# Kernel tuning notes

Hardware: AMD Instinct MI355X
Metric: run time of the kernel (lower is better)

The kernel has to match this reference:

```python
import jax, jax.numpy as jnp
import numpy as np

D_MODEL = 1024
N_HEADS = 16
HEAD_DIM = D_MODEL // N_HEADS  # 64, rope_dim == head_dim
D_FF = 4096
BATCH = 2
SEQ = 2048
EPS = 1e-6


def setup_inputs() -> dict:
    key = jax.random.key(0)
    ks = jax.random.split(key, 12)
    x = jax.random.normal(ks[0], (BATCH, SEQ, D_MODEL), dtype=jnp.float32)
    # realistic RoPE angles: theta = pos * inv_freq, duplicated to fill rope_dim
    half = HEAD_DIM // 2
    inv_freq = 1.0 / (10000.0 ** (jnp.arange(0, half, dtype=jnp.float32) / half))
    pos = jnp.arange(SEQ, dtype=jnp.float32)
    freqs = pos[:, None] * inv_freq[None, :]              # [S, half]
    rotary_pos_emb = jnp.concatenate([freqs, freqs], axis=-1)[:, None, :]  # [S,1,64]
    s = D_MODEL ** -0.5
    wq = jax.random.normal(ks[1], (D_MODEL, D_MODEL), dtype=jnp.float32) * s
    wk = jax.random.normal(ks[2], (D_MODEL, D_MODEL), dtype=jnp.float32) * s
    wv = jax.random.normal(ks[3], (D_MODEL, D_MODEL), dtype=jnp.float32) * s
    wo = jax.random.normal(ks[4], (D_MODEL, D_MODEL), dtype=jnp.float32) * s
    w_gate = jax.random.normal(ks[5], (D_FF, D_MODEL), dtype=jnp.float32) * s
    w_up = jax.random.normal(ks[6], (D_FF, D_MODEL), dtype=jnp.float32) * s
    w_down = jax.random.normal(ks[7], (D_MODEL, D_FF), dtype=jnp.float32) * (D_FF ** -0.5)
    norm1_w = jnp.ones((D_MODEL,), dtype=jnp.float32)
    norm2_w = jnp.ones((D_MODEL,), dtype=jnp.float32)
    return {"x": x, "rotary_pos_emb": rotary_pos_emb, "wq": wq, "wk": wk,
            "wv": wv, "wo": wo, "w_gate": w_gate, "w_up": w_up,
            "w_down": w_down, "norm1_w": norm1_w, "norm2_w": norm2_w}


def _rms_norm(x, w):
    # torch: x / (||x||/sqrt(d) + eps) * w  (eps added to the norm, not variance)
    norm = jnp.linalg.norm(x, axis=-1, keepdims=True) * (x.shape[-1] ** -0.5)
    return x / (norm + EPS) * w


def _rotate_half(t):
    t1, t2 = jnp.split(t, 2, axis=-1)
    return jnp.concatenate([-t2, t1], axis=-1)


def _apply_rope(t, cos, sin):
    # t: [B,H,S,D]; cos/sin: [S,D] broadcast over batch/heads
    return t * cos[None, None] + _rotate_half(t) * sin[None, None]


def reference(x, rotary_pos_emb, wq, wk, wv, wo, w_gate, w_up, w_down, norm1_w, norm2_w):
    B, S, _ = x.shape
    H, D = N_HEADS, HEAD_DIM

    # ---- attention sublayer ----
    residual = x
    h = _rms_norm(x, norm1_w)
    q = (h @ wq.T).reshape(B, S, H, D).transpose(0, 2, 1, 3)  # [B,H,S,D]
    k = (h @ wk.T).reshape(B, S, H, D).transpose(0, 2, 1, 3)
    v = (h @ wv.T).reshape(B, S, H, D).transpose(0, 2, 1, 3)

    freqs = rotary_pos_emb[:, 0, :]  # [S, D] (rope_dim == head_dim)
    cos, sin = jnp.cos(freqs), jnp.sin(freqs)
    q = _apply_rope(q, cos, sin)
    k = _apply_rope(k, cos, sin)

    scores = jnp.einsum('bhsd,bhtd->bhst', q, k) / jnp.sqrt(jnp.float32(D))
    causal = jnp.tril(jnp.ones((S, S), dtype=bool))  # True = keep
    scores = jnp.where(causal[None, None], scores, jnp.finfo(scores.dtype).min)
    attn = jax.nn.softmax(scores, axis=-1)  # dropout is identity in eval
    attn_out = jnp.einsum('bhst,bhtd->bhsd', attn, v)
    attn_out = attn_out.transpose(0, 2, 1, 3).reshape(B, S, H * D)
    x = residual + attn_out @ wo.T

    # ---- SwiGLU MLP sublayer ----
    residual = x
    h = _rms_norm(x, norm2_w)
    gate = h @ w_gate.T
    up = h @ w_up.T
    ff = (jax.nn.silu(gate) * up) @ w_down.T
    return residual + ff
```

## Files before the change

kernel.cpp:

```cpp
#include <hip/hip_runtime.h>

typedef __bf16 bf16;
typedef __attribute__((ext_vector_type(8))) __bf16 bf16x8;
typedef __attribute__((ext_vector_type(4))) float f32x4;

#define B_SZ 2
#define SEQ 2048
#define DM 1024
#define NH 16
#define HD 64
#define DFF 4096
#define NROWS (B_SZ*SEQ)

__device__ __forceinline__ f32x4 mfma16(bf16x8 a, bf16x8 b, f32x4 c) {
    return __builtin_amdgcn_mfma_f32_16x16x32_bf16(a, b, c, 0, 0, 0);
}

__device__ __forceinline__ void gload16(const bf16* g, bf16* l) {
    __builtin_amdgcn_global_load_lds(
        (const __attribute__((address_space(1))) void*)g,
        (__attribute__((address_space(3))) void*)l, 16, 0, 0);
}


__global__ __launch_bounds__(256) void convert_all_k(
    const float* __restrict__ wq, const float* __restrict__ wk,
    const float* __restrict__ wv, const float* __restrict__ wo,
    const float* __restrict__ wg, const float* __restrict__ wu,
    const float* __restrict__ wd,
    bf16* __restrict__ wqkvb, bf16* __restrict__ wob,
    bf16* __restrict__ wgub, bf16* __restrict__ wdb) {
    const long M1 = 1l << 20;
    long i = ((long)blockIdx.x * 256 + threadIdx.x) * 8;
    const float* src; bf16* dst; long off;
    if (i < 3 * M1) {
        int sct = (int)(i >> 20);
        src = sct == 0 ? wq : (sct == 1 ? wk : wv);
        off = i & (M1 - 1); dst = wqkvb + i;
    } else if (i < 4 * M1) {
        src = wo; off = i - 3 * M1; dst = wob + off;
    } else if (i < 12 * M1) {
        long j = i - 4 * M1;
        int fr = (int)(j >> 10), c = (int)(j & 1023);
        int b = fr >> 8, half = (fr >> 7) & 1, f = (b << 7) | (fr & 127);
        src = half ? wu : wg; off = (long)f * 1024 + c; dst = wgub + j;
    } else {
        src = wd; off = i - 12 * M1; dst = wdb + off;
    }
    float4 v0 = *(const float4*)(src + off);
    float4 v1 = *(const float4*)(src + off + 4);
    dst[0] = (bf16)v0.x; dst[1] = (bf16)v0.y; dst[2] = (bf16)v0.z; dst[3] = (bf16)v0.w;
    dst[4] = (bf16)v1.x; dst[5] = (bf16)v1.y; dst[6] = (bf16)v1.z; dst[7] = (bf16)v1.w;
}

__global__ __launch_bounds__(256) void rope_table_k(const float* __restrict__ rope,
                                                    float* __restrict__ ct,
                                                    float* __restrict__ st) {
    int i = blockIdx.x * 256 + threadIdx.x;
    int sI = i >> 5, d = i & 31;
    float f = rope[sI * 64 + d];
    ct[i] = cosf(f);
    st[i] = sinf(f);
}

__global__ __launch_bounds__(256) void rmsnorm_k(const float* __restrict__ x,
                                                 const float* __restrict__ w,
                                                 bf16* __restrict__ o) {
    int row = blockIdx.x;
    int tid = threadIdx.x;
    float4 v = ((const float4*)(x + (long)row * DM))[tid];
    float ss = v.x*v.x + v.y*v.y + v.z*v.z + v.w*v.w;
    #pragma unroll
    for (int off = 32; off >= 1; off >>= 1) ss += __shfl_xor(ss, off, 64);
    __shared__ float sred[4];
    if ((tid & 63) == 0) sred[tid >> 6] = ss;
    __syncthreads();
    float tot = sred[0] + sred[1] + sred[2] + sred[3];
    float scale = 1.f / (sqrtf(tot * (1.f / (float)DM)) + 1e-6f);
    float4 wv = ((const float4*)w)[tid];
    bf16* orow = o + (long)row * DM + tid * 4;
    orow[0] = (bf16)(v.x * scale * wv.x);
    orow[1] = (bf16)(v.y * scale * wv.y);
    orow[2] = (bf16)(v.z * scale * wv.z);
    orow[3] = (bf16)(v.w * scale * wv.w);
}


template<int EPI>
__global__ __launch_bounds__(512, 2)
void gemm256(const bf16* __restrict__ A, const bf16* __restrict__ W,
             int K, bf16* __restrict__ o1, bf16* __restrict__ o2,
             bf16* __restrict__ o3,
             const float* __restrict__ ct, const float* __restrict__ st) {
    __shared__ __align__(16) char smem[131072];
    bf16* Ah = (bf16*)smem;
    bf16* Bh = (bf16*)(smem + 65536);
    const int tid = threadIdx.x;
    const int wid = tid >> 6, l = tid & 63;
    const int lr = l & 15, lg = l >> 4;
    const int wr = wid >> 2, wcn = wid & 3;
    const int nwg = gridDim.x * gridDim.y;
    const int orig = blockIdx.y * gridDim.x + blockIdx.x;
    const int swz = (orig & 7) * (nwg >> 3) + (orig >> 3);
    const int bx = swz % gridDim.x, by = swz / gridDim.x;
    const long mbase = (long)bx * 256;
    const long nbase = (long)by * 256;

    f32x4 acc[8][4] = {};
    const int nk = K >> 6;
    const int P = nk * 2;

    const int aoff0 = lr * 64 + ((wr * 4 + lg) ^ (lr & 7)) * 8;
    const int boff0 = ((wcn & 1) * 64 + lr) * 64 + (((wcn >> 1) * 4 + lg) ^ (lr & 7)) * 8;

    auto stageHalf = [&](int ph) {
        const int d = (ph >> 1) & 1, h = ph & 1, kt = ph >> 1;
        bf16* abase = Ah + (d * 2 + h) * 8192;
        bf16* bbase = Bh + (d * 2 + h) * 8192;
        const long kcol = (long)kt * 64 + h * 32;
        #pragma unroll
        for (int i = 0; i < 2; ++i) {
            int s = i * 512 + tid;
            int prow = s >> 3, pblk = s & 7;
            int L = pblk ^ (prow & 7);
            long gr = (long)((L >> 2) * 128 + prow);
            long gc = kcol + (L & 3) * 8;
            gload16(&A[(mbase + gr) * K + gc], abase + s * 8);
            gload16(&W[(nbase + gr) * K + gc], bbase + s * 8);
        }
    };

    auto computeHalf = [&](int ph) {
        const int d = (ph >> 1) & 1, h = ph & 1;
        const bf16* abase = Ah + (d * 2 + h) * 8192;
        const bf16* bbase = Bh + (d * 2 + h) * 8192;
        bf16x8 bfr[4];
        #pragma unroll
        for (int ni = 0; ni < 4; ++ni)
            bfr[ni] = *(const bf16x8*)&bbase[ni * 1024 + boff0];
        #pragma unroll
        for (int ms = 0; ms < 2; ++ms) {
            bf16x8 af[4];
            #pragma unroll
            for (int mi = 0; mi < 4; ++mi)
                af[mi] = *(const bf16x8*)&abase[(ms * 4 + mi) * 1024 + aoff0];
            __builtin_amdgcn_s_setprio(1);
            #pragma unroll
            for (int mi = 0; mi < 4; ++mi)
                #pragma unroll
                for (int ni = 0; ni < 4; ++ni)
                    acc[ms * 4 + mi][ni] = mfma16(af[mi], bfr[ni], acc[ms * 4 + mi][ni]);
            __builtin_amdgcn_s_setprio(0);
        }
    };

    stageHalf(0);
    stageHalf(1);
    for (int p = 0; p < P; ++p) {
        if (p + 2 < P) stageHalf(p + 2);
        if (p < P - 2)       asm volatile("s_waitcnt vmcnt(8)" ::: "memory");
        else if (p == P - 2) asm volatile("s_waitcnt vmcnt(4)" ::: "memory");
        else                 asm volatile("s_waitcnt vmcnt(0)" ::: "memory");
        __builtin_amdgcn_s_barrier();
        __builtin_amdgcn_sched_barrier(0);
        computeHalf(p);
    }

    if (EPI == 0) {
        const long colW = nbase + wcn * 64;
        const int sect = (int)(colW >> 10);
        const int hh = (int)((colW >> 6) & 15);
        #pragma unroll
        for (int a = 0; a < 8; ++a) {
            #pragma unroll
            for (int nn = 0; nn < 2; ++nn) {
                const int dd = nn * 16 + lr;
                #pragma unroll
                for (int r = 0; r < 4; ++r) {
                    long row = mbase + wr * 128 + a * 16 + 4 * lg + r;
                    int b = (int)(row >> 11), s = (int)(row & 2047);
                    float v1 = acc[a][nn][r];
                    float v2 = acc[a][nn + 2][r];
                    if (sect < 2) {
                        float c = ct[s * 32 + dd], sn = st[s * 32 + dd];
                        bf16* dst = (sect == 0) ? o1 : o2;
                        long pth = (((long)(b * NH + hh) * SEQ + s) << 6) + dd;
                        dst[pth]      = (bf16)(v1 * c - v2 * sn);
                        dst[pth + 32] = (bf16)(v2 * c + v1 * sn);
                    } else {
                        long pth = ((long)(b * NH + hh) * HD + dd) * SEQ + s;
                        o3[pth]            = (bf16)v1;
                        o3[pth + 32 * SEQ] = (bf16)v2;
                    }
                }
            }
        }
    }

    if (EPI == 3) {
        const int fbase = (int)(nbase >> 1);
        bf16* Gl = (bf16*)smem;
        __syncthreads();
        if (wcn < 2) {
            #pragma unroll
            for (int a = 0; a < 8; ++a)
                #pragma unroll
                for (int ni = 0; ni < 4; ++ni)
                    #pragma unroll
                    for (int r = 0; r < 4; ++r) {
                        int grow = wr * 128 + a * 16 + 4 * lg + r;
                        int fc = wcn * 64 + ni * 16 + lr;
                        Gl[grow * 132 + fc] = (bf16)acc[a][ni][r];
                    }
        }
        __syncthreads();
        if (wcn >= 2) {
            #pragma unroll
            for (int a = 0; a < 8; ++a)
                #pragma unroll
                for (int ni = 0; ni < 4; ++ni)
                    #pragma unroll
                    for (int r = 0; r < 4; ++r) {
                        int grow = wr * 128 + a * 16 + 4 * lg + r;
                        int fc = (wcn - 2) * 64 + ni * 16 + lr;
                        float g = (float)Gl[grow * 132 + fc];
                        float u = acc[a][ni][r];
                        float sg = g / (1.f + __expf(-g));
                        long row = mbase + grow;
                        o1[row * 4096 + fbase + fc] = (bf16)(sg * u);
                    }
        }
    }
}


__global__ __launch_bounds__(512, 4)
void gemm64x128(const bf16* __restrict__ A, const bf16* __restrict__ W,
                int K, int N, const float* __restrict__ resid, float* __restrict__ of) {
    __shared__ bf16 As[2][64 * 64];
    __shared__ bf16 Bs[2][128 * 64];
    const int tid = threadIdx.x;
    const int wid = tid >> 6, l = tid & 63;
    const int lr = l & 15, lg = l >> 4;
    const int wr = wid >> 2, wcn = wid & 3;
    const long mbase = (long)blockIdx.x * 64;
    const long nbase = (long)blockIdx.y * 128;

    f32x4 acc[2][2] = {};
    const int nk = K >> 6;

    auto stage = [&](int b, int kt) {
        {
            int s = tid;
            int row = s >> 3, c8 = (s & 7) << 3;
            gload16(&A[(mbase + row) * K + kt * 64 + c8], &As[b][s * 8]);
        }
        #pragma unroll
        for (int i = 0; i < 2; ++i) {
            int s = i * 512 + tid;
            int row = s >> 3, c8 = (s & 7) << 3;
            gload16(&W[(nbase + row) * K + kt * 64 + c8], &Bs[b][s * 8]);
        }
    };
    auto compute = [&](int b) {
        #pragma unroll
        for (int kk = 0; kk < 2; ++kk) {
            bf16x8 af[2], bfr[2];
            #pragma unroll
            for (int mi = 0; mi < 2; ++mi)
                af[mi] = *(const bf16x8*)&As[b][(wr * 32 + mi * 16 + lr) * 64 + kk * 32 + lg * 8];
            #pragma unroll
            for (int ni = 0; ni < 2; ++ni)
                bfr[ni] = *(const bf16x8*)&Bs[b][(wcn * 32 + ni * 16 + lr) * 64 + kk * 32 + lg * 8];
            #pragma unroll
            for (int mi = 0; mi < 2; ++mi)
                #pragma unroll
                for (int ni = 0; ni < 2; ++ni)
                    acc[mi][ni] = mfma16(af[mi], bfr[ni], acc[mi][ni]);
        }
    };

    stage(0, 0);
    __syncthreads();
    int cur = 0;
    for (int kt = 0; kt < nk - 1; ++kt) {
        stage(cur ^ 1, kt + 1);
        compute(cur);
        __syncthreads();
        cur ^= 1;
    }
    compute(cur);

    #pragma unroll
    for (int mi = 0; mi < 2; ++mi)
        #pragma unroll
        for (int ni = 0; ni < 2; ++ni)
            #pragma unroll
            for (int r = 0; r < 4; ++r) {
                long row = mbase + wr * 32 + mi * 16 + 4 * lg + r;
                long col = nbase + wcn * 32 + ni * 16 + lr;
                of[row * N + col] = resid[row * N + col] + acc[mi][ni][r];
            }
}


__device__ __forceinline__ void attn_tile(
    int tb, int qw, bool diag,
    const bf16x8& qf0, const bf16x8& qf1,
    const bf16* Kl, const bf16* Vl, bf16* Plw,
    int lr, int lg, f32x4* oacc, float* mr, f32x4& lacc)
{
    f32x4 s[4];
    __builtin_amdgcn_s_setprio(1);
    #pragma unroll
    for (int tf = 0; tf < 4; ++tf) {
        f32x4 z = {0.f, 0.f, 0.f, 0.f};
        bf16x8 k0 = *(const bf16x8*)&Kl[(tf * 16 + lr) * 64 + ((0 + lg) ^ (lr & 7)) * 8];
        bf16x8 k1 = *(const bf16x8*)&Kl[(tf * 16 + lr) * 64 + ((4 + lg) ^ (lr & 7)) * 8];
        z = mfma16(qf0, k0, z);
        z = mfma16(qf1, k1, z);
        s[tf] = z;
    }
    __builtin_amdgcn_s_setprio(0);

    float pv[4][4];
    float pmax[4] = {-1e30f, -1e30f, -1e30f, -1e30f};
    #pragma unroll
    for (int tf = 0; tf < 4; ++tf) {
        int t = tb + tf * 16 + lr;
        #pragma unroll
        for (int r = 0; r < 4; ++r) {
            float sv = s[tf][r] * 0.125f;
            if (diag && t > qw + 4 * lg + r) sv = -1e30f;
            pv[tf][r] = sv;
            pmax[r] = fmaxf(pmax[r], sv);
        }
    }
    #pragma unroll
    for (int r = 0; r < 4; ++r) {
        pmax[r] = fmaxf(pmax[r], __shfl_xor(pmax[r], 8, 64));
        pmax[r] = fmaxf(pmax[r], __shfl_xor(pmax[r], 4, 64));
        pmax[r] = fmaxf(pmax[r], __shfl_xor(pmax[r], 2, 64));
        pmax[r] = fmaxf(pmax[r], __shfl_xor(pmax[r], 1, 64));
    }
    float alpha[4];
    #pragma unroll
    for (int r = 0; r < 4; ++r) {
        float mn = fmaxf(mr[r], pmax[r]);
        alpha[r] = __expf(mr[r] - mn);
        mr[r] = mn;
    }
    #pragma unroll
    for (int tf = 0; tf < 4; ++tf)
        #pragma unroll
        for (int r = 0; r < 4; ++r)
            Plw[(4 * lg + r) * 68 + tf * 16 + lr] = (bf16)__expf(pv[tf][r] - mr[r]);

    #pragma unroll
    for (int r = 0; r < 4; ++r) lacc[r] *= alpha[r];
    #pragma unroll
    for (int df = 0; df < 4; ++df) {
        f32x4 t4 = oacc[df];
        t4[0] *= alpha[0]; t4[1] *= alpha[1];
        t4[2] *= alpha[2]; t4[3] *= alpha[3];
        oacc[df] = t4;
    }
    bf16x8 pa0, pa1;
    #pragma unroll
    for (int j = 0; j < 8; ++j) {
        pa0[j] = Plw[lr * 68 + lg * 8 + j];
        pa1[j] = Plw[lr * 68 + 32 + lg * 8 + j];
    }
    bf16x8 ones;
    #pragma unroll
    for (int j = 0; j < 8; ++j) ones[j] = (bf16)1.0f;
    __builtin_amdgcn_s_setprio(1);
    lacc = mfma16(pa0, ones, lacc);
    lacc = mfma16(pa1, ones, lacc);
    #pragma unroll
    for (int df = 0; df < 4; ++df) {
        bf16x8 v0 = *(const bf16x8*)&Vl[(df * 16 + lr) * 64 + ((0 + lg) ^ (lr & 7)) * 8];
        bf16x8 v1 = *(const bf16x8*)&Vl[(df * 16 + lr) * 64 + ((4 + lg) ^ (lr & 7)) * 8];
        oacc[df] = mfma16(pa0, v0, oacc[df]);
        oacc[df] = mfma16(pa1, v1, oacc[df]);
    }
    __builtin_amdgcn_s_setprio(0);
}

__global__ __launch_bounds__(256)
void attn_fwd(const bf16* __restrict__ q, const bf16* __restrict__ k,
              const bf16* __restrict__ vt, bf16* __restrict__ o) {
    __shared__ bf16 Kl[2][64 * 64];
    __shared__ bf16 Vl[2][64 * 64];
    __shared__ bf16 Pl[4][16 * 68];
    const int tid = threadIdx.x, wid = tid >> 6, l = tid & 63;
    const int lr = l & 15, lg = l >> 4;
    const int qtA = blockIdx.x;
    const int qtB = 31 - qtA;
    const int bh = blockIdx.y;
    const long kbase = (long)bh * SEQ * HD;
    const long vbase = (long)bh * HD * SEQ;
    const int qwA = qtA * 64 + wid * 16;
    const int qwB = qtB * 64 + wid * 16;

    bf16x8 qA0, qA1, qB0, qB1;
    {
        const bf16* qp = q + kbase + (long)(qwA + lr) * HD + lg * 8;
        qA0 = *(const bf16x8*)qp; qA1 = *(const bf16x8*)(qp + 32);
        const bf16* qp2 = q + kbase + (long)(qwB + lr) * HD + lg * 8;
        qB0 = *(const bf16x8*)qp2; qB1 = *(const bf16x8*)(qp2 + 32);
    }
    f32x4 oA[4] = {}, oB[4] = {};
    f32x4 lA = {0.f, 0.f, 0.f, 0.f}, lB = {0.f, 0.f, 0.f, 0.f};
    float mA[4] = {-1e30f, -1e30f, -1e30f, -1e30f};
    float mB[4] = {-1e30f, -1e30f, -1e30f, -1e30f};

    auto stageKV = [&](int b, int tb) {
        #pragma unroll
        for (int i = 0; i < 4; ++i) {
            int slot = i * 256 + tid;
            int row = (slot >> 3) & 63;
            int bs = (slot & 7) ^ (row & 7);
            if (slot < 512)
                gload16(&k[kbase + (long)(tb + row) * HD + bs * 8], &Kl[b][slot * 8]);
            else
                gload16(&vt[vbase + (long)row * SEQ + tb + bs * 8], &Vl[b][(slot - 512) * 8]);
        }
    };

    const int nt = qtB + 1;
    stageKV(0, 0);
    __syncthreads();
    int cur = 0;
    for (int tb_i = 0; tb_i < nt; ++tb_i) {
        const int tb = tb_i * 64;
        if (tb_i + 1 < nt) stageKV(cur ^ 1, tb + 64);
        if (tb_i <= qtA)
            attn_tile(tb, qwA, tb_i == qtA, qA0, qA1, Kl[cur], Vl[cur], Pl[wid], lr, lg, oA, mA, lA);
        attn_tile(tb, qwB, tb_i == qtB, qB0, qB1, Kl[cur], Vl[cur], Pl[wid], lr, lg, oB, mB, lB);
        __syncthreads();
        cur ^= 1;
    }

    const int b = bh >> 4, h = bh & 15;
    #pragma unroll
    for (int df = 0; df < 4; ++df) {
        #pragma unroll
        for (int r = 0; r < 4; ++r) {
            int sA = qwA + 4 * lg + r;
            int sB = qwB + 4 * lg + r;
            o[((long)(b * SEQ + sA) * DM) + h * HD + df * 16 + lr] = (bf16)(oA[df][r] / lA[r]);
            o[((long)(b * SEQ + sB) * DM) + h * HD + df * 16 + lr] = (bf16)(oB[df][r] / lB[r]);
        }
    }
}


extern "C" void kernel_launch(void* const* d_in, const int* in_sizes, int n_in,
                              void* d_out, int out_size, void* d_ws, size_t ws_size,
                              hipStream_t stream) {
    (void)in_sizes; (void)n_in; (void)out_size; (void)ws_size;
    const float* x    = (const float*)d_in[0];
    const float* rope = (const float*)d_in[1];
    const float* wq   = (const float*)d_in[2];
    const float* wk   = (const float*)d_in[3];
    const float* wv   = (const float*)d_in[4];
    const float* wo   = (const float*)d_in[5];
    const float* wg   = (const float*)d_in[6];
    const float* wu   = (const float*)d_in[7];
    const float* wd   = (const float*)d_in[8];
    const float* n1w  = (const float*)d_in[9];
    const float* n2w  = (const float*)d_in[10];
    float* out = (float*)d_out;

    char* ws = (char*)d_ws;
    const size_t MB = 1u << 20;
    bf16* wqkvb = (bf16*)(ws + 0 * MB);
    bf16* wob   = (bf16*)(ws + 6 * MB);
    bf16* wgub  = (bf16*)(ws + 8 * MB);
    bf16* wdb   = (bf16*)(ws + 24 * MB);
    bf16* hb    = (bf16*)(ws + 32 * MB);
    bf16* qb_   = (bf16*)(ws + 40 * MB);
    bf16* kb_   = (bf16*)(ws + 56 * MB);
    bf16* vtb   = (bf16*)(ws + 72 * MB);
    bf16* attnb = (bf16*)(ws + 88 * MB);
    float* x2   = (float*)(ws + 40 * MB);
    bf16* midb  = (bf16*)(ws + 56 * MB);
    float* ctab = (float*)(ws + 104 * MB);
    float* stab = (float*)(ws + 104 * MB + (1u << 18));

    convert_all_k<<<8192, 256, 0, stream>>>(wq, wk, wv, wo, wg, wu, wd,
                                            wqkvb, wob, wgub, wdb);
    rope_table_k<<<256, 256, 0, stream>>>(rope, ctab, stab);

    rmsnorm_k<<<NROWS, 256, 0, stream>>>(x, n1w, hb);

    gemm256<0><<<dim3(16, 12), 512, 0, stream>>>(hb, wqkvb, DM, qb_, kb_, vtb, ctab, stab);

    attn_fwd<<<dim3(16, 32), 256, 0, stream>>>(qb_, kb_, vtb, attnb);

    gemm64x128<<<dim3(64, 8), 512, 0, stream>>>(attnb, wob, DM, DM, x, x2);

    rmsnorm_k<<<NROWS, 256, 0, stream>>>(x2, n2w, hb);

    gemm256<3><<<dim3(16, 32), 512, 0, stream>>>(hb, wgub, DM, midb, nullptr, nullptr, nullptr, nullptr);

    gemm64x128<<<dim3(64, 8), 512, 0, stream>>>(midb, wdb, DFF, DM, x2, out);
}
```

Baseline: 331.8 us.

## Deepen GEMM pipelines, swizzle LDS in small GEMM, interleave gate/up rows

The big GEMM moves from a 2-ahead to a 3-ahead staging of K half-tiles across four LDS buffers, issuing the next load after the barrier. The gate/up weight packing is re-interleaved in 32-row groups so each wave holds matching gate and up columns, which lets the SwiGLU epilogue run in registers without the LDS round-trip and two syncthreads. The 64x128 GEMM gains a triple-buffered LDS pipeline with explicit vmcnt waits, an XOR-swizzled LDS layout to cut bank conflicts, and setprio around the MFMAs. These changes raise LDS use and rely on hand-counted vmcnt values being correct.

```diff
diff --git a/kernel.cpp b/kernel.cpp
--- a/kernel.cpp
+++ b/kernel.cpp
@@ -42,8 +42,9 @@
     } else if (i < 12 * M1) {
         long j = i - 4 * M1;
         int fr = (int)(j >> 10), c = (int)(j & 1023);
-        int b = fr >> 8, half = (fr >> 7) & 1, f = (b << 7) | (fr & 127);
-        src = half ? wu : wg; off = (long)f * 1024 + c; dst = wgub + j;
+        int g = fr >> 6, r = fr & 63;
+        int f = g * 32 + (r & 31);
+        src = (r & 32) ? wu : wg; off = (long)f * 1024 + c; dst = wgub + j;
     } else {
         src = wd; off = i - 12 * M1; dst = wdb + off;
     }
@@ -114,9 +115,9 @@
     const int boff0 = ((wcn & 1) * 64 + lr) * 64 + (((wcn >> 1) * 4 + lg) ^ (lr & 7)) * 8;
 
     auto stageHalf = [&](int ph) {
-        const int d = (ph >> 1) & 1, h = ph & 1, kt = ph >> 1;
-        bf16* abase = Ah + (d * 2 + h) * 8192;
-        bf16* bbase = Bh + (d * 2 + h) * 8192;
+        const int buf = ph & 3, h = ph & 1, kt = ph >> 1;
+        bf16* abase = Ah + buf * 8192;
+        bf16* bbase = Bh + buf * 8192;
         const long kcol = (long)kt * 64 + h * 32;
         #pragma unroll
         for (int i = 0; i < 2; ++i) {
@@ -131,9 +132,9 @@
     };
 
     auto computeHalf = [&](int ph) {
-        const int d = (ph >> 1) & 1, h = ph & 1;
-        const bf16* abase = Ah + (d * 2 + h) * 8192;
-        const bf16* bbase = Bh + (d * 2 + h) * 8192;
+        const int buf = ph & 3;
+        const bf16* abase = Ah + buf * 8192;
+        const bf16* bbase = Bh + buf * 8192;
         bf16x8 bfr[4];
         #pragma unroll
         for (int ni = 0; ni < 4; ++ni)
@@ -156,13 +157,14 @@
 
     stageHalf(0);
     stageHalf(1);
+    stageHalf(2);
     for (int p = 0; p < P; ++p) {
-        if (p + 2 < P) stageHalf(p + 2);
         if (p < P - 2)       asm volatile("s_waitcnt vmcnt(8)" ::: "memory");
         else if (p == P - 2) asm volatile("s_waitcnt vmcnt(4)" ::: "memory");
         else                 asm volatile("s_waitcnt vmcnt(0)" ::: "memory");
         __builtin_amdgcn_s_barrier();
         __builtin_amdgcn_sched_barrier(0);
+        if (p + 3 < P) stageHalf(p + 3);
         computeHalf(p);
     }
 
@@ -198,38 +200,19 @@
     }
 
     if (EPI == 3) {
-        const int fbase = (int)(nbase >> 1);
-        bf16* Gl = (bf16*)smem;
-        __syncthreads();
-        if (wcn < 2) {
-            #pragma unroll
-            for (int a = 0; a < 8; ++a)
+        const int fb = (int)(nbase + wcn * 64) >> 1;
+        #pragma unroll
+        for (int a = 0; a < 8; ++a)
+            #pragma unroll
+            for (int ni = 0; ni < 2; ++ni)
                 #pragma unroll
-                for (int ni = 0; ni < 4; ++ni)
-                    #pragma unroll
-                    for (int r = 0; r < 4; ++r) {
-                        int grow = wr * 128 + a * 16 + 4 * lg + r;
-                        int fc = wcn * 64 + ni * 16 + lr;
-                        Gl[grow * 132 + fc] = (bf16)acc[a][ni][r];
-                    }
-        }
-        __syncthreads();
-        if (wcn >= 2) {
-            #pragma unroll
-            for (int a = 0; a < 8; ++a)
-                #pragma unroll
-                for (int ni = 0; ni < 4; ++ni)
-                    #pragma unroll
-                    for (int r = 0; r < 4; ++r) {
-                        int grow = wr * 128 + a * 16 + 4 * lg + r;
-                        int fc = (wcn - 2) * 64 + ni * 16 + lr;
-                        float g = (float)Gl[grow * 132 + fc];
-                        float u = acc[a][ni][r];
-                        float sg = g / (1.f + __expf(-g));
-                        long row = mbase + grow;
-                        o1[row * 4096 + fbase + fc] = (bf16)(sg * u);
-                    }
-        }
+                for (int r = 0; r < 4; ++r) {
+                    long row = mbase + wr * 128 + a * 16 + 4 * lg + r;
+                    float g = acc[a][ni][r];
+                    float u = acc[a][ni + 2][r];
+                    float sg = g / (1.f + __expf(-g));
+                    o1[row * 4096 + fb + ni * 16 + lr] = (bf16)(sg * u);
+                }
     }
 }
 
@@ -237,8 +220,8 @@
 __global__ __launch_bounds__(512, 4)
 void gemm64x128(const bf16* __restrict__ A, const bf16* __restrict__ W,
                 int K, int N, const float* __restrict__ resid, float* __restrict__ of) {
-    __shared__ bf16 As[2][64 * 64];
-    __shared__ bf16 Bs[2][128 * 64];
+    __shared__ bf16 As[3][64 * 64];
+    __shared__ bf16 Bs[3][128 * 64];
     const int tid = threadIdx.x;
     const int wid = tid >> 6, l = tid & 63;
     const int lr = l & 15, lg = l >> 4;
@@ -252,14 +235,16 @@
     auto stage = [&](int b, int kt) {
         {
             int s = tid;
-            int row = s >> 3, c8 = (s & 7) << 3;
-            gload16(&A[(mbase + row) * K + kt * 64 + c8], &As[b][s * 8]);
+            int row = s >> 3, pblk = s & 7;
+            int L = pblk ^ (row & 7);
+            gload16(&A[(mbase + row) * K + kt * 64 + L * 8], &As[b][s * 8]);
         }
         #pragma unroll
         for (int i = 0; i < 2; ++i) {
             int s = i * 512 + tid;
-            int row = s >> 3, c8 = (s & 7) << 3;
-            gload16(&W[(nbase + row) * K + kt * 64 + c8], &Bs[b][s * 8]);
+            int row = s >> 3, pblk = s & 7;
+            int L = pblk ^ (row & 7);
+            gload16(&W[(nbase + row) * K + kt * 64 + L * 8], &Bs[b][s * 8]);
         }
     };
     auto compute = [&](int b) {
@@ -267,29 +252,35 @@
         for (int kk = 0; kk < 2; ++kk) {
             bf16x8 af[2], bfr[2];
             #pragma unroll
-            for (int mi = 0; mi < 2; ++mi)
-                af[mi] = *(const bf16x8*)&As[b][(wr * 32 + mi * 16 + lr) * 64 + kk * 32 + lg * 8];
-            #pragma unroll
-            for (int ni = 0; ni < 2; ++ni)
-                bfr[ni] = *(const bf16x8*)&Bs[b][(wcn * 32 + ni * 16 + lr) * 64 + kk * 32 + lg * 8];
+            for (int mi = 0; mi < 2; ++mi) {
+                int row = wr * 32 + mi * 16 + lr;
+                af[mi] = *(const bf16x8*)&As[b][row * 64 + ((kk * 4 + lg) ^ (lr & 7)) * 8];
+            }
+            #pragma unroll
+            for (int ni = 0; ni < 2; ++ni) {
+                int row = wcn * 32 + ni * 16 + lr;
+                bfr[ni] = *(const bf16x8*)&Bs[b][row * 64 + ((kk * 4 + lg) ^ (lr & 7)) * 8];
+            }
+            __builtin_amdgcn_s_setprio(1);
             #pragma unroll
             for (int mi = 0; mi < 2; ++mi)
                 #pragma unroll
                 for (int ni = 0; ni < 2; ++ni)
                     acc[mi][ni] = mfma16(af[mi], bfr[ni], acc[mi][ni]);
+            __builtin_amdgcn_s_setprio(0);
         }
     };
 
     stage(0, 0);
-    __syncthreads();
-    int cur = 0;
-    for (int kt = 0; kt < nk - 1; ++kt) {
-        stage(cur ^ 1, kt + 1);
-        compute(cur);
-        __syncthreads();
-        cur ^= 1;
-    }
-    compute(cur);
+    stage(1, 1);
+    for (int kt = 0; kt < nk; ++kt) {
+        if (kt < nk - 1) asm volatile("s_waitcnt vmcnt(3)" ::: "memory");
+        else             asm volatile("s_waitcnt vmcnt(0)" ::: "memory");
+        __builtin_amdgcn_s_barrier();
+        __builtin_amdgcn_sched_barrier(0);
+        if (kt + 2 < nk) stage((kt + 2) % 3, kt + 2);
+        compute(kt % 3);
+    }
 
     #pragma unroll
     for (int mi = 0; mi < 2; ++mi)
```

Result: faster. 300.3 us (-9.5%).
